# Kernel optimization log

Measured on AMD Instinct MI355X. Metric: run time of the kernel, lower is better.

## Reference

```python
import jax, jax.numpy as jnp
import numpy as np

N_QUBITS = 8
N_LAYERS = 2
LN_EPS = 1e-5


def _ry(theta):
    # RY(t) = [[cos t/2, -sin t/2],[sin t/2, cos t/2]]; works batched or scalar
    c = jnp.cos(theta * 0.5)
    s = jnp.sin(theta * 0.5)
    return jnp.stack([jnp.stack([c, -s], -1), jnp.stack([s, c], -1)], -2).astype(jnp.complex64)


def _rz(theta):
    # RZ(t) = diag(e^{-it/2}, e^{it/2})
    e = jnp.exp(-0.5j * theta.astype(jnp.complex64))
    z = jnp.zeros_like(e)
    return jnp.stack([jnp.stack([e, z], -1), jnp.stack([z, jnp.conj(e)], -1)], -2)


def _apply_1q(psi, U, wire):
    # psi: (B, 2,...,2) with wire 0 most significant (PennyLane convention)
    ax = wire + 1
    psi = jnp.moveaxis(psi, ax, 1)
    psi = jnp.einsum('bpq,bq...->bp...', U, psi)
    return jnp.moveaxis(psi, 1, ax)


def _apply_cnot(psi, c, t):
    ca, ta = c + 1, t + 1
    psi = jnp.moveaxis(psi, (ca, ta), (1, 2))  # (B, 2c, 2t, rest)
    psi = jnp.stack([psi[:, 0], psi[:, 1, ::-1]], axis=1)  # flip target where control=1
    return jnp.moveaxis(psi, (1, 2), (ca, ta))


def _quantum(feats, q_weights):
    # feats: (B, 8) angle-encoded features; q_weights: (2, 8, 3)
    B = feats.shape[0]
    f = feats.astype(jnp.float32)
    psi = jnp.zeros((B,) + (2,) * N_QUBITS, jnp.complex64)
    psi = psi.at[(slice(None),) + (0,) * N_QUBITS].set(1.0)
    for l in range(N_LAYERS):
        for i in range(N_QUBITS):
            # gate order on wire i: RY(f_i), RZ(w0), RY(w1), RZ(w2)
            C = _rz(q_weights[l, i, 2]) @ _ry(q_weights[l, i, 1]) @ _rz(q_weights[l, i, 0])
            U = jnp.einsum('pq,bqr->bpr', C, _ry(f[:, i]))  # (B,2,2)
            psi = _apply_1q(psi, U, i)
        for i in range(N_QUBITS):
            psi = _apply_cnot(psi, i, (i + 1) % N_QUBITS)
    probs = jnp.abs(psi) ** 2  # (B, 2,...,2)
    zs = []
    for i in range(N_QUBITS):
        p = jnp.moveaxis(probs, i + 1, 1).reshape(B, 2, -1).sum(-1)
        zs.append(p[:, 0] - p[:, 1])  # <Z_i> = P(0) - P(1)
    return jnp.stack(zs, -1)  # (B, 8)


def setup_inputs() -> dict:
    key = jax.random.key(0)
    ks = jax.random.split(key, 12)
    B, D, H = 16384, 768, 256
    s = lambda fan_in: 1.0 / np.sqrt(fan_in)
    return {
        'x': jax.random.normal(ks[0], (B, D), jnp.float32),
        'W1': jax.random.uniform(ks[1], (D, H), jnp.float32, -s(D), s(D)),
        'b1': jax.random.uniform(ks[2], (H,), jnp.float32, -s(D), s(D)),
        'W2': jax.random.uniform(ks[3], (H, N_QUBITS), jnp.float32, -s(H), s(H)),
        'b2': jax.random.uniform(ks[4], (N_QUBITS,), jnp.float32, -s(H), s(H)),
        'q_weights': jax.random.normal(ks[5], (N_LAYERS, N_QUBITS, 3), jnp.float32) * 0.01,
        'W3': jax.random.uniform(ks[6], (N_QUBITS, H), jnp.float32, -s(N_QUBITS), s(N_QUBITS)),
        'b3': jax.random.uniform(ks[7], (H,), jnp.float32, -s(N_QUBITS), s(N_QUBITS)),
        'W4': jax.random.uniform(ks[8], (H, D), jnp.float32, -s(H), s(H)),
        'b4': jax.random.uniform(ks[9], (D,), jnp.float32, -s(H), s(H)),
        'gamma': jnp.ones((D,), jnp.float32),
        'beta': jnp.zeros((D,), jnp.float32),
    }


def reference(x, W1, b1, W2, b2, q_weights, W3, b3, W4, b4, gamma, beta):
    # classical compress (dropout = identity in eval)
    h = jax.nn.gelu(x @ W1 + b1, approximate=False)
    feats = h @ W2 + b2  # (B, 8) angle encoding
    z = _quantum(feats, q_weights)  # (B, 8) Pauli-Z expectations
    e = jax.nn.gelu(z @ W3 + b3, approximate=False)
    expanded = e @ W4 + b4
    y = x + expanded
    mu = y.mean(-1, keepdims=True)
    var = y.var(-1, keepdims=True)
    return gamma * (y - mu) / jnp.sqrt(var + LN_EPS) + beta
```

## Files before the change

kernel.cpp:

```cpp
#include <hip/hip_runtime.h>
#include <hip/hip_bf16.h>
#include <math.h>


typedef __attribute__((ext_vector_type(8))) short bf16x8;
typedef __attribute__((ext_vector_type(4))) float f32x4;

__device__ __forceinline__ float gelu_f(float x) {
    return 0.5f * x * (1.0f + erff(x * 0.70710678118654752f));
}

__device__ __forceinline__ short f2b(float x) {
    __hip_bfloat16 h = __float2bfloat16(x);
    return reinterpret_cast<short&>(h);
}

__device__ __forceinline__ short4 f4_to_b4(float4 v) {
    return make_short4(f2b(v.x), f2b(v.y), f2b(v.z), f2b(v.w));
}

__global__ __launch_bounds__(256) void transpose_bf16_kernel(
    const float* __restrict__ in, short* __restrict__ out, int K, int N)
{
    __shared__ float tl[32][33];
    const int k0 = blockIdx.y * 32, n0 = blockIdx.x * 32;
    const int r = threadIdx.x >> 3, c4 = (threadIdx.x & 7) * 4;
    const float4 v = *(const float4*)(in + (size_t)(k0 + r) * N + n0 + c4);
    tl[r][c4] = v.x; tl[r][c4 + 1] = v.y; tl[r][c4 + 2] = v.z; tl[r][c4 + 3] = v.w;
    __syncthreads();
    short4 o = make_short4(f2b(tl[c4][r]), f2b(tl[c4 + 1][r]),
                           f2b(tl[c4 + 2][r]), f2b(tl[c4 + 3][r]));
    *(short4*)(out + (size_t)(n0 + r) * K + k0 + c4) = o;
}

__global__ __launch_bounds__(256) void setup_kernel(
    const float* __restrict__ qw, const float* __restrict__ W2,
    float* __restrict__ Cg, short* __restrict__ W2T)
{
    const int t = threadIdx.x;
    if (t < 16) {
        const float w0 = qw[t * 3 + 0];
        const float w1 = qw[t * 3 + 1];
        const float w2 = qw[t * 3 + 2];
        const float a0 = 0.5f * w0, a2 = 0.5f * w2;
        float s1, c1; sincosf(0.5f * w1, &s1, &c1);
        float sp, cp; sincosf(a0 + a2, &sp, &cp);
        float sm, cm; sincosf(a0 - a2, &sm, &cm);
        Cg[t * 8 + 0] =  c1 * cp;  Cg[t * 8 + 1] = -c1 * sp;
        Cg[t * 8 + 2] = -s1 * cm;  Cg[t * 8 + 3] = -s1 * sm;
        Cg[t * 8 + 4] =  s1 * cm;  Cg[t * 8 + 5] = -s1 * sm;
        Cg[t * 8 + 6] =  c1 * cp;  Cg[t * 8 + 7] =  c1 * sp;
    }
    for (int idx = t; idx < 16 * 256; idx += 256) {
        const int n = idx & 15, k = idx >> 4;
        W2T[(size_t)n * 256 + k] = (n < 8) ? f2b(W2[(size_t)k * 8 + n]) : (short)0;
    }
}

__global__ __launch_bounds__(512) void gemm1_feats_kernel(
    const float* __restrict__ x, const short* __restrict__ W1bt,
    const float* __restrict__ b1, const short* __restrict__ W2T,
    const float* __restrict__ b2, float* __restrict__ feats, int M)
{
    __shared__ short As[2][64][40];
    __shared__ short hb[64][264];

    const int tid = threadIdx.x;
    const int wid = tid >> 6, L = tid & 63;
    const int quad = L >> 4, r16 = L & 15;
    const int mw = wid & 1, nw = wid >> 1;
    const int m0 = blockIdx.x * 64;

    const int m_s = tid >> 3, k_s = (tid & 7) << 2;
    const float* xp = x + (size_t)(m0 + m_s) * 768 + k_s;

    const short* bp = W1bt + (size_t)(nw * 64 + r16) * 768 + quad * 8;

    f32x4 acc[2][4];
    #pragma unroll
    for (int i = 0; i < 2; ++i)
        #pragma unroll
        for (int j = 0; j < 4; ++j) acc[i][j] = (f32x4){0.f, 0.f, 0.f, 0.f};

    float4 v0 = *(const float4*)(xp);
    *(short4*)&As[0][m_s][k_s] = f4_to_b4(v0);
    float4 v1 = *(const float4*)(xp + 32);
    __syncthreads();

    for (int kt = 0; kt < 24; ++kt) {
        const int buf = kt & 1;
        float4 vn = v1;
        if (kt + 2 < 24) vn = *(const float4*)(xp + (kt + 2) * 32);

        const bf16x8 a0 = *(const bf16x8*)&As[buf][32 * mw + r16][quad * 8];
        const bf16x8 a1 = *(const bf16x8*)&As[buf][32 * mw + 16 + r16][quad * 8];
        #pragma unroll
        for (int nt = 0; nt < 4; ++nt) {
            const bf16x8 bfr = *(const bf16x8*)(bp + (size_t)nt * 16 * 768 + kt * 32);
            acc[0][nt] = __builtin_amdgcn_mfma_f32_16x16x32_bf16(a0, bfr, acc[0][nt], 0, 0, 0);
            acc[1][nt] = __builtin_amdgcn_mfma_f32_16x16x32_bf16(a1, bfr, acc[1][nt], 0, 0, 0);
        }
        if (kt + 1 < 24) {
            *(short4*)&As[buf ^ 1][m_s][k_s] = f4_to_b4(v1);
        }
        __syncthreads();
        v1 = vn;
    }

    #pragma unroll
    for (int mt = 0; mt < 2; ++mt) {
        #pragma unroll
        for (int nt = 0; nt < 4; ++nt) {
            const int n = nw * 64 + nt * 16 + r16;
            const float bv = b1[n];
            #pragma unroll
            for (int reg = 0; reg < 4; ++reg) {
                const int rrow = 32 * mw + 16 * mt + quad * 4 + reg;
                hb[rrow][n] = f2b(gelu_f(acc[mt][nt][reg] + bv));
            }
        }
    }
    __syncthreads();

    if (wid < 4) {
        const int mt = wid;
        f32x4 fa = (f32x4){0.f, 0.f, 0.f, 0.f};
        #pragma unroll
        for (int kt = 0; kt < 8; ++kt) {
            const bf16x8 ha = *(const bf16x8*)&hb[16 * mt + r16][kt * 32 + quad * 8];
            const bf16x8 wb = *(const bf16x8*)(W2T + (size_t)r16 * 256 + kt * 32 + quad * 8);
            fa = __builtin_amdgcn_mfma_f32_16x16x32_bf16(ha, wb, fa, 0, 0, 0);
        }
        if (r16 < 8) {
            const float bv = b2[r16];
            #pragma unroll
            for (int reg = 0; reg < 4; ++reg) {
                const int row = m0 + 16 * mt + quad * 4 + reg;
                feats[(size_t)row * 8 + r16] = fa[reg] + bv;
            }
        }
    }
}

__global__ __launch_bounds__(256) void quantum_kernel(
    const float* __restrict__ feats, const float* __restrict__ Cg,
    const float* __restrict__ W3, const float* __restrict__ b3,
    short* __restrict__ ebt)
{
    const int t = threadIdx.x;
    const int wid = t >> 6, L = t & 63;
    const int row = blockIdx.x * 4 + wid;

    const float fv = feats[(size_t)row * 8 + (L & 7)];
    float sv, cv;
    sincosf(0.5f * fv, &sv, &cv);
    float cf[8], sf[8];
    #pragma unroll
    for (int w = 0; w < 8; ++w) {
        cf[w] = __shfl(cv, w, 64);
        sf[w] = __shfl(sv, w, 64);
    }

    float re[4], im[4];
    #pragma unroll
    for (int r = 0; r < 4; ++r) { re[r] = 0.0f; im[r] = 0.0f; }
    re[0] = (L == 0) ? 1.0f : 0.0f;

    const int G = L ^ (L >> 1);
    const int mapB = G ^ 48;
    const bool par = __popc(L) & 1;

    #pragma unroll
    for (int l = 0; l < 2; ++l) {
        #pragma unroll
        for (int w = 0; w < 8; ++w) {
            const float* Cw = Cg + (l * 8 + w) * 8;
            const float c0 = Cw[0], c1 = Cw[1], c2 = Cw[2], c3 = Cw[3];
            const float c4 = Cw[4], c5 = Cw[5], c6 = Cw[6], c7 = Cw[7];
            const float U00r = cf[w]*c0 + sf[w]*c2, U00i = cf[w]*c1 + sf[w]*c3;
            const float U01r = cf[w]*c2 - sf[w]*c0, U01i = cf[w]*c3 - sf[w]*c1;
            const float U10r = cf[w]*c4 + sf[w]*c6, U10i = cf[w]*c5 + sf[w]*c7;
            const float U11r = cf[w]*c6 - sf[w]*c4, U11i = cf[w]*c7 - sf[w]*c5;

            if (w <= 5) {
                const int kb = 5 - w;
                const int xm = 1 << kb;
                const bool hi = (L >> kb) & 1;
                const float u0r = hi ? U11r : U00r;
                const float u0i = hi ? U11i : U00i;
                const float u1r = hi ? U10r : U01r;
                const float u1i = hi ? U10i : U01i;
                #pragma unroll
                for (int r = 0; r < 4; ++r) {
                    const float ore = __shfl_xor(re[r], xm, 64);
                    const float oim = __shfl_xor(im[r], xm, 64);
                    const float nre = u0r*re[r] - u0i*im[r] + u1r*ore - u1i*oim;
                    const float nim = u0r*im[r] + u0i*re[r] + u1r*oim + u1i*ore;
                    re[r] = nre; im[r] = nim;
                }
            } else if (w == 6) {
                float nre[4], nim[4];
                #pragma unroll
                for (int p = 0; p < 2; ++p) {
                    nre[p]   = U00r*re[p]-U00i*im[p] + U01r*re[p+2]-U01i*im[p+2];
                    nim[p]   = U00r*im[p]+U00i*re[p] + U01r*im[p+2]+U01i*re[p+2];
                    nre[p+2] = U10r*re[p]-U10i*im[p] + U11r*re[p+2]-U11i*im[p+2];
                    nim[p+2] = U10r*im[p]+U10i*re[p] + U11r*im[p+2]+U11i*re[p+2];
                }
                #pragma unroll
                for (int r = 0; r < 4; ++r) { re[r] = nre[r]; im[r] = nim[r]; }
            } else {
                float nre[4], nim[4];
                #pragma unroll
                for (int p = 0; p < 4; p += 2) {
                    nre[p]   = U00r*re[p]-U00i*im[p] + U01r*re[p+1]-U01i*im[p+1];
                    nim[p]   = U00r*im[p]+U00i*re[p] + U01r*im[p+1]+U01i*re[p+1];
                    nre[p+1] = U10r*re[p]-U10i*im[p] + U11r*re[p+1]-U11i*im[p+1];
                    nim[p+1] = U10r*im[p]+U10i*re[p] + U11r*im[p+1]+U11i*re[p+1];
                }
                #pragma unroll
                for (int r = 0; r < 4; ++r) { re[r] = nre[r]; im[r] = nim[r]; }
            }
        }

        {
            const float s0r = par ? re[2] : re[0], s0i = par ? im[2] : im[0];
            const float s1r = par ? re[3] : re[1], s1i = par ? im[3] : im[1];
            const float s2r = par ? re[1] : re[3], s2i = par ? im[1] : im[3];
            const float s3r = par ? re[0] : re[2], s3i = par ? im[0] : im[2];
            re[0] = __shfl(s0r, G, 64);    im[0] = __shfl(s0i, G, 64);
            re[1] = __shfl(s1r, mapB, 64); im[1] = __shfl(s1i, mapB, 64);
            re[2] = __shfl(s2r, G, 64);    im[2] = __shfl(s2i, G, 64);
            re[3] = __shfl(s3r, mapB, 64); im[3] = __shfl(s3i, mapB, 64);
        }
    }

    const float p0 = re[0]*re[0] + im[0]*im[0];
    const float p1 = re[1]*re[1] + im[1]*im[1];
    const float p2 = re[2]*re[2] + im[2]*im[2];
    const float p3 = re[3]*re[3] + im[3]*im[3];
    const float pt = p0 + p1 + p2 + p3;
    float v[8];
    #pragma unroll
    for (int w = 0; w < 6; ++w) v[w] = ((L >> (5 - w)) & 1) ? -pt : pt;
    v[6] = p0 + p1 - p2 - p3;
    v[7] = p0 - p1 + p2 - p3;
    #pragma unroll
    for (int j = 0; j < 4; ++j) {
        const float send = (L & 1) ? v[j] : v[j + 4];
        const float keep = (L & 1) ? v[j + 4] : v[j];
        v[j] = keep + __shfl_xor(send, 1, 64);
    }
    #pragma unroll
    for (int j = 0; j < 2; ++j) {
        const float send = (L & 2) ? v[j] : v[j + 2];
        const float keep = (L & 2) ? v[j + 2] : v[j];
        v[j] = keep + __shfl_xor(send, 2, 64);
    }
    {
        const float send = (L & 4) ? v[0] : v[1];
        const float keep = (L & 4) ? v[1] : v[0];
        v[0] = keep + __shfl_xor(send, 4, 64);
    }
    v[0] += __shfl_xor(v[0], 8, 64);
    v[0] += __shfl_xor(v[0], 16, 64);
    v[0] += __shfl_xor(v[0], 32, 64);
    float z[8];
    #pragma unroll
    for (int w = 0; w < 8; ++w) {
        const int src = ((w & 1) << 2) | (w & 2) | ((w >> 2) & 1);
        z[w] = __shfl(v[0], src, 64);
    }

    const float4 b3v = *(const float4*)(b3 + 4 * L);
    float acc[4] = {b3v.x, b3v.y, b3v.z, b3v.w};
    #pragma unroll
    for (int w = 0; w < 8; ++w) {
        const float4 w3v = *(const float4*)(W3 + (size_t)w * 256 + 4 * L);
        acc[0] += z[w] * w3v.x; acc[1] += z[w] * w3v.y;
        acc[2] += z[w] * w3v.z; acc[3] += z[w] * w3v.w;
    }
    *(short4*)(ebt + (size_t)row * 256 + 4 * L) =
        make_short4(f2b(gelu_f(acc[0])), f2b(gelu_f(acc[1])),
                    f2b(gelu_f(acc[2])), f2b(gelu_f(acc[3])));
}

__global__ __launch_bounds__(256) void gemm4_ln_kernel(
    const short* __restrict__ ebt, const short* __restrict__ W4bt,
    const float* __restrict__ b4, const float* __restrict__ x,
    const float* __restrict__ gamma, const float* __restrict__ beta,
    float* __restrict__ out, int M)
{
    __shared__ short Ae[16][264];
    __shared__ float red[4][16][2];
    __shared__ float stats[16][2];

    const int tid = threadIdx.x;
    const int wv = tid >> 6, L = tid & 63;
    const int quad = L >> 4, r16 = L & 15;
    const int m0 = blockIdx.x * 16;
    const int n0 = wv * 192;

    {
        const int m_s = tid >> 4, k16 = (tid & 15) * 16;
        const int4* ep = (const int4*)(ebt + (size_t)(m0 + m_s) * 256 + k16);
        const int4 e0 = ep[0], e1 = ep[1];
        *(int4*)&Ae[m_s][k16] = e0;
        *(int4*)&Ae[m_s][k16 + 8] = e1;
    }
    __syncthreads();

    const short* bp = W4bt + (size_t)(n0 + r16) * 256 + quad * 8;

    f32x4 acc[12];
    #pragma unroll
    for (int nt = 0; nt < 12; ++nt) acc[nt] = (f32x4){0.f, 0.f, 0.f, 0.f};

    for (int kt = 0; kt < 8; ++kt) {
        const bf16x8 af = *(const bf16x8*)&Ae[r16][kt * 32 + quad * 8];
        #pragma unroll
        for (int nt = 0; nt < 12; ++nt) {
            const bf16x8 bfr = *(const bf16x8*)(bp + (size_t)nt * 16 * 256 + kt * 32);
            acc[nt] = __builtin_amdgcn_mfma_f32_16x16x32_bf16(af, bfr, acc[nt], 0, 0, 0);
        }
    }

    float ps[4] = {0.f, 0.f, 0.f, 0.f}, pq[4] = {0.f, 0.f, 0.f, 0.f};
    #pragma unroll
    for (int nt = 0; nt < 12; ++nt) {
        const int n = n0 + nt * 16 + r16;
        const float bv = b4[n];
        #pragma unroll
        for (int reg = 0; reg < 4; ++reg) {
            const int row = m0 + quad * 4 + reg;
            const float y = acc[nt][reg] + bv + x[(size_t)row * 768 + n];
            acc[nt][reg] = y;
            ps[reg] += y;
            pq[reg] += y * y;
        }
    }
    #pragma unroll
    for (int off = 1; off < 16; off <<= 1) {
        #pragma unroll
        for (int reg = 0; reg < 4; ++reg) {
            ps[reg] += __shfl_xor(ps[reg], off, 64);
            pq[reg] += __shfl_xor(pq[reg], off, 64);
        }
    }
    if (r16 == 0) {
        #pragma unroll
        for (int reg = 0; reg < 4; ++reg) {
            red[wv][quad * 4 + reg][0] = ps[reg];
            red[wv][quad * 4 + reg][1] = pq[reg];
        }
    }
    __syncthreads();
    if (tid < 16) {
        const float S = red[0][tid][0] + red[1][tid][0] + red[2][tid][0] + red[3][tid][0];
        const float Q = red[0][tid][1] + red[1][tid][1] + red[2][tid][1] + red[3][tid][1];
        const float mu = S * (1.0f / 768.0f);
        const float var = Q * (1.0f / 768.0f) - mu * mu;
        stats[tid][0] = mu;
        stats[tid][1] = rsqrtf(var + 1e-5f);
    }
    __syncthreads();

    float mu_r[4], rs_r[4];
    #pragma unroll
    for (int reg = 0; reg < 4; ++reg) {
        mu_r[reg] = stats[quad * 4 + reg][0];
        rs_r[reg] = stats[quad * 4 + reg][1];
    }
    #pragma unroll
    for (int nt = 0; nt < 12; ++nt) {
        const int n = n0 + nt * 16 + r16;
        const float g = gamma[n], bt = beta[n];
        #pragma unroll
        for (int reg = 0; reg < 4; ++reg) {
            const int row = m0 + quad * 4 + reg;
            out[(size_t)row * 768 + n] = g * (acc[nt][reg] - mu_r[reg]) * rs_r[reg] + bt;
        }
    }
}

extern "C" void kernel_launch(void* const* d_in, const int* in_sizes, int n_in,
                              void* d_out, int out_size, void* d_ws, size_t ws_size,
                              hipStream_t stream) {
    (void)n_in; (void)out_size; (void)ws_size;
    const float* x     = (const float*)d_in[0];
    const float* W1    = (const float*)d_in[1];
    const float* b1    = (const float*)d_in[2];
    const float* W2    = (const float*)d_in[3];
    const float* b2    = (const float*)d_in[4];
    const float* qw    = (const float*)d_in[5];
    const float* W3    = (const float*)d_in[6];
    const float* b3    = (const float*)d_in[7];
    const float* W4    = (const float*)d_in[8];
    const float* b4    = (const float*)d_in[9];
    const float* gamma = (const float*)d_in[10];
    const float* beta  = (const float*)d_in[11];
    float* out = (float*)d_out;

    const int D = 768, H = 256;
    const int B = in_sizes[0] / D;

    short* W1bt  = (short*)d_ws;
    short* W4bt  = W1bt + (size_t)H * D;
    short* W2T   = W4bt + (size_t)D * H;
    float* Cg    = (float*)(W2T + 16 * 256);
    float* feats = Cg + 128;
    short* ebt   = (short*)(feats + (size_t)B * 8);

    transpose_bf16_kernel<<<dim3(H / 32, D / 32), 256, 0, stream>>>(W1, W1bt, D, H);
    transpose_bf16_kernel<<<dim3(D / 32, H / 32), 256, 0, stream>>>(W4, W4bt, H, D);
    setup_kernel<<<1, 256, 0, stream>>>(qw, W2, Cg, W2T);
    gemm1_feats_kernel<<<dim3(B / 64), 512, 0, stream>>>(x, W1bt, b1, W2T, b2, feats, B);
    quantum_kernel<<<dim3(B / 4), 256, 0, stream>>>(feats, Cg, W3, b3, ebt);
    gemm4_ln_kernel<<<dim3(B / 16), 256, 0, stream>>>(ebt, W4bt, b4, x, gamma, beta, out, B);
}
```

Before: 234.1 us.

## Fuse GEMM1, quantum simulation, GEMM4 and LayerNorm into one kernel with split-bf16 activations

Measured after the change: 209.4 us. -10.6%, faster.

```diff
diff --git a/kernel.cpp b/kernel.cpp
--- a/kernel.cpp
+++ b/kernel.cpp
@@ -15,114 +15,153 @@
     return reinterpret_cast<short&>(h);
 }
 
+__device__ __forceinline__ float b2f(short s) {
+    union { unsigned u; float f; } c;
+    c.u = ((unsigned)(unsigned short)s) << 16;
+    return c.f;
+}
+
 __device__ __forceinline__ short4 f4_to_b4(float4 v) {
     return make_short4(f2b(v.x), f2b(v.y), f2b(v.z), f2b(v.w));
 }
 
-__global__ __launch_bounds__(256) void transpose_bf16_kernel(
-    const float* __restrict__ in, short* __restrict__ out, int K, int N)
+__device__ __forceinline__ void split4(float4 v, short4& hi, short4& lo) {
+    hi = f4_to_b4(v);
+    lo = make_short4(f2b(v.x - b2f(hi.x)), f2b(v.y - b2f(hi.y)),
+                     f2b(v.z - b2f(hi.z)), f2b(v.w - b2f(hi.w)));
+}
+
+__global__ __launch_bounds__(256) void prep_kernel(
+    const float* __restrict__ W1, const float* __restrict__ W4,
+    const float* __restrict__ qw, const float* __restrict__ W2,
+    short* __restrict__ W1bt, short* __restrict__ W4bt,
+    short* __restrict__ W2T, float* __restrict__ Cg)
 {
     __shared__ float tl[32][33];
-    const int k0 = blockIdx.y * 32, n0 = blockIdx.x * 32;
-    const int r = threadIdx.x >> 3, c4 = (threadIdx.x & 7) * 4;
-    const float4 v = *(const float4*)(in + (size_t)(k0 + r) * N + n0 + c4);
-    tl[r][c4] = v.x; tl[r][c4 + 1] = v.y; tl[r][c4 + 2] = v.z; tl[r][c4 + 3] = v.w;
-    __syncthreads();
-    short4 o = make_short4(f2b(tl[c4][r]), f2b(tl[c4 + 1][r]),
-                           f2b(tl[c4 + 2][r]), f2b(tl[c4 + 3][r]));
-    *(short4*)(out + (size_t)(n0 + r) * K + k0 + c4) = o;
-}
-
-__global__ __launch_bounds__(256) void setup_kernel(
-    const float* __restrict__ qw, const float* __restrict__ W2,
-    float* __restrict__ Cg, short* __restrict__ W2T)
-{
-    const int t = threadIdx.x;
-    if (t < 16) {
-        const float w0 = qw[t * 3 + 0];
-        const float w1 = qw[t * 3 + 1];
-        const float w2 = qw[t * 3 + 2];
-        const float a0 = 0.5f * w0, a2 = 0.5f * w2;
-        float s1, c1; sincosf(0.5f * w1, &s1, &c1);
-        float sp, cp; sincosf(a0 + a2, &sp, &cp);
-        float sm, cm; sincosf(a0 - a2, &sm, &cm);
-        Cg[t * 8 + 0] =  c1 * cp;  Cg[t * 8 + 1] = -c1 * sp;
-        Cg[t * 8 + 2] = -s1 * cm;  Cg[t * 8 + 3] = -s1 * sm;
-        Cg[t * 8 + 4] =  s1 * cm;  Cg[t * 8 + 5] = -s1 * sm;
-        Cg[t * 8 + 6] =  c1 * cp;  Cg[t * 8 + 7] =  c1 * sp;
+    const int i = blockIdx.x, t = threadIdx.x;
+    if (i < 384) {
+        const float* in; short* outp; int K, N, k0, n0;
+        if (i < 192) {
+            in = W1; outp = W1bt; K = 768; N = 256;
+            k0 = (i >> 3) * 32; n0 = (i & 7) * 32;
+        } else {
+            const int j = i - 192;
+            in = W4; outp = W4bt; K = 256; N = 768;
+            k0 = (j & 7) * 32; n0 = (j >> 3) * 32;
+        }
+        const int r = t >> 3, c4 = (t & 7) * 4;
+        const float4 v = *(const float4*)(in + (size_t)(k0 + r) * N + n0 + c4);
+        tl[r][c4] = v.x; tl[r][c4 + 1] = v.y; tl[r][c4 + 2] = v.z; tl[r][c4 + 3] = v.w;
+        __syncthreads();
+        short4 o = make_short4(f2b(tl[c4][r]), f2b(tl[c4 + 1][r]),
+                               f2b(tl[c4 + 2][r]), f2b(tl[c4 + 3][r]));
+        *(short4*)(outp + (size_t)(n0 + r) * K + k0 + c4) = o;
+    } else {
+        if (t < 16) {
+            const float w0 = qw[t * 3 + 0];
+            const float w1 = qw[t * 3 + 1];
+            const float w2 = qw[t * 3 + 2];
+            const float a0 = 0.5f * w0, a2 = 0.5f * w2;
+            float s1, c1; sincosf(0.5f * w1, &s1, &c1);
+            float sp, cp; sincosf(a0 + a2, &sp, &cp);
+            float sm, cm; sincosf(a0 - a2, &sm, &cm);
+            Cg[t * 8 + 0] =  c1 * cp;  Cg[t * 8 + 1] = -c1 * sp;
+            Cg[t * 8 + 2] = -s1 * cm;  Cg[t * 8 + 3] = -s1 * sm;
+            Cg[t * 8 + 4] =  s1 * cm;  Cg[t * 8 + 5] = -s1 * sm;
+            Cg[t * 8 + 6] =  c1 * cp;  Cg[t * 8 + 7] =  c1 * sp;
+        }
+        for (int idx = t; idx < 16 * 256; idx += 256) {
+            const int n = idx & 15, k = idx >> 4;
+            W2T[(size_t)n * 256 + k] = (n < 8) ? f2b(W2[(size_t)k * 8 + n]) : (short)0;
+        }
     }
-    for (int idx = t; idx < 16 * 256; idx += 256) {
-        const int n = idx & 15, k = idx >> 4;
-        W2T[(size_t)n * 256 + k] = (n < 8) ? f2b(W2[(size_t)k * 8 + n]) : (short)0;
-    }
-}
-
-__global__ __launch_bounds__(512) void gemm1_feats_kernel(
+}
+
+__global__ __launch_bounds__(256, 2) void fused_kernel(
     const float* __restrict__ x, const short* __restrict__ W1bt,
     const float* __restrict__ b1, const short* __restrict__ W2T,
-    const float* __restrict__ b2, float* __restrict__ feats, int M)
+    const float* __restrict__ b2, const float* __restrict__ Cg,
+    const float* __restrict__ W3, const float* __restrict__ b3,
+    const short* __restrict__ W4bt, const float* __restrict__ b4,
+    const float* __restrict__ gamma, const float* __restrict__ beta,
+    float* __restrict__ out)
 {
-    __shared__ short As[2][64][40];
-    __shared__ short hb[64][264];
+    __shared__ short Ash[2][32][40];
+    __shared__ short Asl[2][32][40];
+    __shared__ short hb[32][264];
+    __shared__ short ehi[32][264];
+    __shared__ short elo[32][264];
+    __shared__ float feats_s[32][8];
+    __shared__ float red[4][32][2];
+    __shared__ float stats_s[32][2];
 
     const int tid = threadIdx.x;
     const int wid = tid >> 6, L = tid & 63;
     const int quad = L >> 4, r16 = L & 15;
-    const int mw = wid & 1, nw = wid >> 1;
-    const int m0 = blockIdx.x * 64;
-
-    const int m_s = tid >> 3, k_s = (tid & 7) << 2;
-    const float* xp = x + (size_t)(m0 + m_s) * 768 + k_s;
-
-    const short* bp = W1bt + (size_t)(nw * 64 + r16) * 768 + quad * 8;
-
-    f32x4 acc[2][4];
-    #pragma unroll
-    for (int i = 0; i < 2; ++i)
-        #pragma unroll
-        for (int j = 0; j < 4; ++j) acc[i][j] = (f32x4){0.f, 0.f, 0.f, 0.f};
-
-    float4 v0 = *(const float4*)(xp);
-    *(short4*)&As[0][m_s][k_s] = f4_to_b4(v0);
-    float4 v1 = *(const float4*)(xp + 32);
-    __syncthreads();
-
-    for (int kt = 0; kt < 24; ++kt) {
-        const int buf = kt & 1;
-        float4 vn = v1;
-        if (kt + 2 < 24) vn = *(const float4*)(xp + (kt + 2) * 32);
-
-        const bf16x8 a0 = *(const bf16x8*)&As[buf][32 * mw + r16][quad * 8];
-        const bf16x8 a1 = *(const bf16x8*)&As[buf][32 * mw + 16 + r16][quad * 8];
-        #pragma unroll
-        for (int nt = 0; nt < 4; ++nt) {
-            const bf16x8 bfr = *(const bf16x8*)(bp + (size_t)nt * 16 * 768 + kt * 32);
-            acc[0][nt] = __builtin_amdgcn_mfma_f32_16x16x32_bf16(a0, bfr, acc[0][nt], 0, 0, 0);
-            acc[1][nt] = __builtin_amdgcn_mfma_f32_16x16x32_bf16(a1, bfr, acc[1][nt], 0, 0, 0);
-        }
-        if (kt + 1 < 24) {
-            *(short4*)&As[buf ^ 1][m_s][k_s] = f4_to_b4(v1);
-        }
+    const int m0 = blockIdx.x * 32;
+
+    {
+        const int m_s = tid >> 3, k_s = (tid & 7) << 2;
+        const float* xp = x + (size_t)(m0 + m_s) * 768 + k_s;
+        const short* bp = W1bt + (size_t)(wid * 64 + r16) * 768 + quad * 8;
+
+        f32x4 acc[2][4];
+        #pragma unroll
+        for (int i = 0; i < 2; ++i)
+            #pragma unroll
+            for (int j = 0; j < 4; ++j) acc[i][j] = (f32x4){0.f, 0.f, 0.f, 0.f};
+
+        float4 v0 = *(const float4*)(xp);
+        {
+            short4 hi, lo; split4(v0, hi, lo);
+            *(short4*)&Ash[0][m_s][k_s] = hi;
+            *(short4*)&Asl[0][m_s][k_s] = lo;
+        }
+        float4 v1 = *(const float4*)(xp + 32);
         __syncthreads();
-        v1 = vn;
-    }
-
-    #pragma unroll
-    for (int mt = 0; mt < 2; ++mt) {
-        #pragma unroll
-        for (int nt = 0; nt < 4; ++nt) {
-            const int n = nw * 64 + nt * 16 + r16;
-            const float bv = b1[n];
-            #pragma unroll
-            for (int reg = 0; reg < 4; ++reg) {
-                const int rrow = 32 * mw + 16 * mt + quad * 4 + reg;
-                hb[rrow][n] = f2b(gelu_f(acc[mt][nt][reg] + bv));
+
+        for (int kt = 0; kt < 24; ++kt) {
+            const int buf = kt & 1;
+            float4 vn = v1;
+            if (kt + 2 < 24) vn = *(const float4*)(xp + (kt + 2) * 32);
+
+            const bf16x8 a0h = *(const bf16x8*)&Ash[buf][r16][quad * 8];
+            const bf16x8 a0l = *(const bf16x8*)&Asl[buf][r16][quad * 8];
+            const bf16x8 a1h = *(const bf16x8*)&Ash[buf][16 + r16][quad * 8];
+            const bf16x8 a1l = *(const bf16x8*)&Asl[buf][16 + r16][quad * 8];
+            #pragma unroll
+            for (int nt = 0; nt < 4; ++nt) {
+                const bf16x8 bfr = *(const bf16x8*)(bp + (size_t)nt * 16 * 768 + kt * 32);
+                acc[0][nt] = __builtin_amdgcn_mfma_f32_16x16x32_bf16(a0h, bfr, acc[0][nt], 0, 0, 0);
+                acc[0][nt] = __builtin_amdgcn_mfma_f32_16x16x32_bf16(a0l, bfr, acc[0][nt], 0, 0, 0);
+                acc[1][nt] = __builtin_amdgcn_mfma_f32_16x16x32_bf16(a1h, bfr, acc[1][nt], 0, 0, 0);
+                acc[1][nt] = __builtin_amdgcn_mfma_f32_16x16x32_bf16(a1l, bfr, acc[1][nt], 0, 0, 0);
+            }
+            if (kt + 1 < 24) {
+                short4 hi, lo; split4(v1, hi, lo);
+                *(short4*)&Ash[buf ^ 1][m_s][k_s] = hi;
+                *(short4*)&Asl[buf ^ 1][m_s][k_s] = lo;
+            }
+            __syncthreads();
+            v1 = vn;
+        }
+
+        #pragma unroll
+        for (int mt = 0; mt < 2; ++mt) {
+            #pragma unroll
+            for (int nt = 0; nt < 4; ++nt) {
+                const int n = wid * 64 + nt * 16 + r16;
+                const float bv = b1[n];
+                #pragma unroll
+                for (int reg = 0; reg < 4; ++reg) {
+                    hb[16 * mt + quad * 4 + reg][n] = f2b(gelu_f(acc[mt][nt][reg] + bv));
+                }
             }
         }
     }
     __syncthreads();
 
-    if (wid < 4) {
+    if (wid < 2) {
         const int mt = wid;
         f32x4 fa = (f32x4){0.f, 0.f, 0.f, 0.f};
         #pragma unroll
@@ -135,250 +174,254 @@
             const float bv = b2[r16];
             #pragma unroll
             for (int reg = 0; reg < 4; ++reg) {
-                const int row = m0 + 16 * mt + quad * 4 + reg;
-                feats[(size_t)row * 8 + r16] = fa[reg] + bv;
-            }
-        }
-    }
-}
-
-__global__ __launch_bounds__(256) void quantum_kernel(
-    const float* __restrict__ feats, const float* __restrict__ Cg,
-    const float* __restrict__ W3, const float* __restrict__ b3,
-    short* __restrict__ ebt)
-{
-    const int t = threadIdx.x;
-    const int wid = t >> 6, L = t & 63;
-    const int row = blockIdx.x * 4 + wid;
-
-    const float fv = feats[(size_t)row * 8 + (L & 7)];
-    float sv, cv;
-    sincosf(0.5f * fv, &sv, &cv);
-    float cf[8], sf[8];
-    #pragma unroll
-    for (int w = 0; w < 8; ++w) {
-        cf[w] = __shfl(cv, w, 64);
-        sf[w] = __shfl(sv, w, 64);
-    }
-
-    float re[4], im[4];
-    #pragma unroll
-    for (int r = 0; r < 4; ++r) { re[r] = 0.0f; im[r] = 0.0f; }
-    re[0] = (L == 0) ? 1.0f : 0.0f;
-
-    const int G = L ^ (L >> 1);
-    const int mapB = G ^ 48;
-    const bool par = __popc(L) & 1;
-
-    #pragma unroll
-    for (int l = 0; l < 2; ++l) {
-        #pragma unroll
-        for (int w = 0; w < 8; ++w) {
-            const float* Cw = Cg + (l * 8 + w) * 8;
-            const float c0 = Cw[0], c1 = Cw[1], c2 = Cw[2], c3 = Cw[3];
-            const float c4 = Cw[4], c5 = Cw[5], c6 = Cw[6], c7 = Cw[7];
-            const float U00r = cf[w]*c0 + sf[w]*c2, U00i = cf[w]*c1 + sf[w]*c3;
-            const float U01r = cf[w]*c2 - sf[w]*c0, U01i = cf[w]*c3 - sf[w]*c1;
-            const float U10r = cf[w]*c4 + sf[w]*c6, U10i = cf[w]*c5 + sf[w]*c7;
-            const float U11r = cf[w]*c6 - sf[w]*c4, U11i = cf[w]*c7 - sf[w]*c5;
-
-            if (w <= 5) {
-                const int kb = 5 - w;
-                const int xm = 1 << kb;
-                const bool hi = (L >> kb) & 1;
-                const float u0r = hi ? U11r : U00r;
-                const float u0i = hi ? U11i : U00i;
-                const float u1r = hi ? U10r : U01r;
-                const float u1i = hi ? U10i : U01i;
-                #pragma unroll
-                for (int r = 0; r < 4; ++r) {
-                    const float ore = __shfl_xor(re[r], xm, 64);
-                    const float oim = __shfl_xor(im[r], xm, 64);
-                    const float nre = u0r*re[r] - u0i*im[r] + u1r*ore - u1i*oim;
-                    const float nim = u0r*im[r] + u0i*re[r] + u1r*oim + u1i*ore;
-                    re[r] = nre; im[r] = nim;
-                }
-            } else if (w == 6) {
-                float nre[4], nim[4];
-                #pragma unroll
-                for (int p = 0; p < 2; ++p) {
-                    nre[p]   = U00r*re[p]-U00i*im[p] + U01r*re[p+2]-U01i*im[p+2];
-                    nim[p]   = U00r*im[p]+U00i*re[p] + U01r*im[p+2]+U01i*re[p+2];
-                    nre[p+2] = U10r*re[p]-U10i*im[p] + U11r*re[p+2]-U11i*im[p+2];
-                    nim[p+2] = U10r*im[p]+U10i*re[p] + U11r*im[p+2]+U11i*re[p+2];
-                }
-                #pragma unroll
-                for (int r = 0; r < 4; ++r) { re[r] = nre[r]; im[r] = nim[r]; }
-            } else {
-                float nre[4], nim[4];
-                #pragma unroll
-                for (int p = 0; p < 4; p += 2) {
-                    nre[p]   = U00r*re[p]-U00i*im[p] + U01r*re[p+1]-U01i*im[p+1];
-                    nim[p]   = U00r*im[p]+U00i*re[p] + U01r*im[p+1]+U01i*re[p+1];
-                    nre[p+1] = U10r*re[p]-U10i*im[p] + U11r*re[p+1]-U11i*im[p+1];
-                    nim[p+1] = U10r*im[p]+U10i*re[p] + U11r*im[p+1]+U11i*re[p+1];
-                }
-                #pragma unroll
-                for (int r = 0; r < 4; ++r) { re[r] = nre[r]; im[r] = nim[r]; }
-            }
-        }
-
-        {
-            const float s0r = par ? re[2] : re[0], s0i = par ? im[2] : im[0];
-            const float s1r = par ? re[3] : re[1], s1i = par ? im[3] : im[1];
-            const float s2r = par ? re[1] : re[3], s2i = par ? im[1] : im[3];
-            const float s3r = par ? re[0] : re[2], s3i = par ? im[0] : im[2];
-            re[0] = __shfl(s0r, G, 64);    im[0] = __shfl(s0i, G, 64);
-            re[1] = __shfl(s1r, mapB, 64); im[1] = __shfl(s1i, mapB, 64);
-            re[2] = __shfl(s2r, G, 64);    im[2] = __shfl(s2i, G, 64);
-            re[3] = __shfl(s3r, mapB, 64); im[3] = __shfl(s3i, mapB, 64);
-        }
-    }
-
-    const float p0 = re[0]*re[0] + im[0]*im[0];
-    const float p1 = re[1]*re[1] + im[1]*im[1];
-    const float p2 = re[2]*re[2] + im[2]*im[2];
-    const float p3 = re[3]*re[3] + im[3]*im[3];
-    const float pt = p0 + p1 + p2 + p3;
-    float v[8];
-    #pragma unroll
-    for (int w = 0; w < 6; ++w) v[w] = ((L >> (5 - w)) & 1) ? -pt : pt;
-    v[6] = p0 + p1 - p2 - p3;
-    v[7] = p0 - p1 + p2 - p3;
-    #pragma unroll
-    for (int j = 0; j < 4; ++j) {
-        const float send = (L & 1) ? v[j] : v[j + 4];
-        const float keep = (L & 1) ? v[j + 4] : v[j];
-        v[j] = keep + __shfl_xor(send, 1, 64);
-    }
-    #pragma unroll
-    for (int j = 0; j < 2; ++j) {
-        const float send = (L & 2) ? v[j] : v[j + 2];
-        const float keep = (L & 2) ? v[j + 2] : v[j];
-        v[j] = keep + __shfl_xor(send, 2, 64);
-    }
-    {
-        const float send = (L & 4) ? v[0] : v[1];
-        const float keep = (L & 4) ? v[1] : v[0];
-        v[0] = keep + __shfl_xor(send, 4, 64);
-    }
-    v[0] += __shfl_xor(v[0], 8, 64);
-    v[0] += __shfl_xor(v[0], 16, 64);
-    v[0] += __shfl_xor(v[0], 32, 64);
-    float z[8];
-    #pragma unroll
-    for (int w = 0; w < 8; ++w) {
-        const int src = ((w & 1) << 2) | (w & 2) | ((w >> 2) & 1);
-        z[w] = __shfl(v[0], src, 64);
-    }
-
-    const float4 b3v = *(const float4*)(b3 + 4 * L);
-    float acc[4] = {b3v.x, b3v.y, b3v.z, b3v.w};
-    #pragma unroll
-    for (int w = 0; w < 8; ++w) {
-        const float4 w3v = *(const float4*)(W3 + (size_t)w * 256 + 4 * L);
-        acc[0] += z[w] * w3v.x; acc[1] += z[w] * w3v.y;
-        acc[2] += z[w] * w3v.z; acc[3] += z[w] * w3v.w;
-    }
-    *(short4*)(ebt + (size_t)row * 256 + 4 * L) =
-        make_short4(f2b(gelu_f(acc[0])), f2b(gelu_f(acc[1])),
-                    f2b(gelu_f(acc[2])), f2b(gelu_f(acc[3])));
-}
-
-__global__ __launch_bounds__(256) void gemm4_ln_kernel(
-    const short* __restrict__ ebt, const short* __restrict__ W4bt,
-    const float* __restrict__ b4, const float* __restrict__ x,
-    const float* __restrict__ gamma, const float* __restrict__ beta,
-    float* __restrict__ out, int M)
-{
-    __shared__ short Ae[16][264];
-    __shared__ float red[4][16][2];
-    __shared__ float stats[16][2];
-
-    const int tid = threadIdx.x;
-    const int wv = tid >> 6, L = tid & 63;
-    const int quad = L >> 4, r16 = L & 15;
-    const int m0 = blockIdx.x * 16;
-    const int n0 = wv * 192;
-
-    {
-        const int m_s = tid >> 4, k16 = (tid & 15) * 16;
-        const int4* ep = (const int4*)(ebt + (size_t)(m0 + m_s) * 256 + k16);
-        const int4 e0 = ep[0], e1 = ep[1];
-        *(int4*)&Ae[m_s][k16] = e0;
-        *(int4*)&Ae[m_s][k16 + 8] = e1;
+                feats_s[16 * mt + quad * 4 + reg][r16] = fa[reg] + bv;
+            }
+        }
     }
     __syncthreads();
 
-    const short* bp = W4bt + (size_t)(n0 + r16) * 256 + quad * 8;
-
-    f32x4 acc[12];
-    #pragma unroll
-    for (int nt = 0; nt < 12; ++nt) acc[nt] = (f32x4){0.f, 0.f, 0.f, 0.f};
-
-    for (int kt = 0; kt < 8; ++kt) {
-        const bf16x8 af = *(const bf16x8*)&Ae[r16][kt * 32 + quad * 8];
-        #pragma unroll
-        for (int nt = 0; nt < 12; ++nt) {
-            const bf16x8 bfr = *(const bf16x8*)(bp + (size_t)nt * 16 * 256 + kt * 32);
-            acc[nt] = __builtin_amdgcn_mfma_f32_16x16x32_bf16(af, bfr, acc[nt], 0, 0, 0);
-        }
-    }
-
-    float ps[4] = {0.f, 0.f, 0.f, 0.f}, pq[4] = {0.f, 0.f, 0.f, 0.f};
-    #pragma unroll
-    for (int nt = 0; nt < 12; ++nt) {
-        const int n = n0 + nt * 16 + r16;
-        const float bv = b4[n];
-        #pragma unroll
-        for (int reg = 0; reg < 4; ++reg) {
-            const int row = m0 + quad * 4 + reg;
-            const float y = acc[nt][reg] + bv + x[(size_t)row * 768 + n];
-            acc[nt][reg] = y;
-            ps[reg] += y;
-            pq[reg] += y * y;
-        }
-    }
-    #pragma unroll
-    for (int off = 1; off < 16; off <<= 1) {
-        #pragma unroll
-        for (int reg = 0; reg < 4; ++reg) {
-            ps[reg] += __shfl_xor(ps[reg], off, 64);
-            pq[reg] += __shfl_xor(pq[reg], off, 64);
-        }
-    }
-    if (r16 == 0) {
-        #pragma unroll
-        for (int reg = 0; reg < 4; ++reg) {
-            red[wv][quad * 4 + reg][0] = ps[reg];
-            red[wv][quad * 4 + reg][1] = pq[reg];
+    {
+        float4 w3r[8];
+        #pragma unroll
+        for (int w = 0; w < 8; ++w) w3r[w] = *(const float4*)(W3 + (size_t)w * 256 + 4 * L);
+        const float4 b3v = *(const float4*)(b3 + 4 * L);
+
+        const int G = L ^ (L >> 1);
+        const int mapB = G ^ 48;
+        const bool par = __popc(L) & 1;
+
+        #pragma unroll 1
+        for (int rr = 0; rr < 8; ++rr) {
+            const int row = wid * 8 + rr;
+            const float fv = feats_s[row][L & 7];
+            float sv, cv;
+            sincosf(0.5f * fv, &sv, &cv);
+            float cf[8], sf[8];
+            #pragma unroll
+            for (int w = 0; w < 8; ++w) {
+                cf[w] = __shfl(cv, w, 64);
+                sf[w] = __shfl(sv, w, 64);
+            }
+
+            float re[4], im[4];
+            #pragma unroll
+            for (int r = 0; r < 4; ++r) { re[r] = 0.0f; im[r] = 0.0f; }
+            re[0] = (L == 0) ? 1.0f : 0.0f;
+
+            #pragma unroll
+            for (int l = 0; l < 2; ++l) {
+                #pragma unroll
+                for (int w = 0; w < 8; ++w) {
+                    const float* Cw = Cg + (l * 8 + w) * 8;
+                    const float c0 = Cw[0], c1 = Cw[1], c2 = Cw[2], c3 = Cw[3];
+                    const float c4 = Cw[4], c5 = Cw[5], c6 = Cw[6], c7 = Cw[7];
+                    const float U00r = cf[w]*c0 + sf[w]*c2, U00i = cf[w]*c1 + sf[w]*c3;
+                    const float U01r = cf[w]*c2 - sf[w]*c0, U01i = cf[w]*c3 - sf[w]*c1;
+                    const float U10r = cf[w]*c4 + sf[w]*c6, U10i = cf[w]*c5 + sf[w]*c7;
+                    const float U11r = cf[w]*c6 - sf[w]*c4, U11i = cf[w]*c7 - sf[w]*c5;
+
+                    if (w <= 5) {
+                        const int kb = 5 - w;
+                        const int xm = 1 << kb;
+                        const bool hi = (L >> kb) & 1;
+                        const float u0r = hi ? U11r : U00r;
+                        const float u0i = hi ? U11i : U00i;
+                        const float u1r = hi ? U10r : U01r;
+                        const float u1i = hi ? U10i : U01i;
+                        #pragma unroll
+                        for (int r = 0; r < 4; ++r) {
+                            const float ore = __shfl_xor(re[r], xm, 64);
+                            const float oim = __shfl_xor(im[r], xm, 64);
+                            const float nre = u0r*re[r] - u0i*im[r] + u1r*ore - u1i*oim;
+                            const float nim = u0r*im[r] + u0i*re[r] + u1r*oim + u1i*ore;
+                            re[r] = nre; im[r] = nim;
+                        }
+                    } else if (w == 6) {
+                        float nre[4], nim[4];
+                        #pragma unroll
+                        for (int p = 0; p < 2; ++p) {
+                            nre[p]   = U00r*re[p]-U00i*im[p] + U01r*re[p+2]-U01i*im[p+2];
+                            nim[p]   = U00r*im[p]+U00i*re[p] + U01r*im[p+2]+U01i*re[p+2];
+                            nre[p+2] = U10r*re[p]-U10i*im[p] + U11r*re[p+2]-U11i*im[p+2];
+                            nim[p+2] = U10r*im[p]+U10i*re[p] + U11r*im[p+2]+U11i*re[p+2];
+                        }
+                        #pragma unroll
+                        for (int r = 0; r < 4; ++r) { re[r] = nre[r]; im[r] = nim[r]; }
+                    } else {
+                        float nre[4], nim[4];
+                        #pragma unroll
+                        for (int p = 0; p < 4; p += 2) {
+                            nre[p]   = U00r*re[p]-U00i*im[p] + U01r*re[p+1]-U01i*im[p+1];
+                            nim[p]   = U00r*im[p]+U00i*re[p] + U01r*im[p+1]+U01i*re[p+1];
+                            nre[p+1] = U10r*re[p]-U10i*im[p] + U11r*re[p+1]-U11i*im[p+1];
+                            nim[p+1] = U10r*im[p]+U10i*re[p] + U11r*im[p+1]+U11i*re[p+1];
+                        }
+                        #pragma unroll
+                        for (int r = 0; r < 4; ++r) { re[r] = nre[r]; im[r] = nim[r]; }
+                    }
+                }
+
+                {
+                    const float s0r = par ? re[2] : re[0], s0i = par ? im[2] : im[0];
+                    const float s1r = par ? re[3] : re[1], s1i = par ? im[3] : im[1];
+                    const float s2r = par ? re[1] : re[3], s2i = par ? im[1] : im[3];
+                    const float s3r = par ? re[0] : re[2], s3i = par ? im[0] : im[2];
+                    re[0] = __shfl(s0r, G, 64);    im[0] = __shfl(s0i, G, 64);
+                    re[1] = __shfl(s1r, mapB, 64); im[1] = __shfl(s1i, mapB, 64);
+                    re[2] = __shfl(s2r, G, 64);    im[2] = __shfl(s2i, G, 64);
+                    re[3] = __shfl(s3r, mapB, 64); im[3] = __shfl(s3i, mapB, 64);
+                }
+            }
+
+            const float p0 = re[0]*re[0] + im[0]*im[0];
+            const float p1 = re[1]*re[1] + im[1]*im[1];
+            const float p2 = re[2]*re[2] + im[2]*im[2];
+            const float p3 = re[3]*re[3] + im[3]*im[3];
+            const float pt = p0 + p1 + p2 + p3;
+            float v[8];
+            #pragma unroll
+            for (int w = 0; w < 6; ++w) v[w] = ((L >> (5 - w)) & 1) ? -pt : pt;
+            v[6] = p0 + p1 - p2 - p3;
+            v[7] = p0 - p1 + p2 - p3;
+            #pragma unroll
+            for (int j = 0; j < 4; ++j) {
+                const float send = (L & 1) ? v[j] : v[j + 4];
+                const float keep = (L & 1) ? v[j + 4] : v[j];
+                v[j] = keep + __shfl_xor(send, 1, 64);
+            }
+            #pragma unroll
+            for (int j = 0; j < 2; ++j) {
+                const float send = (L & 2) ? v[j] : v[j + 2];
+                const float keep = (L & 2) ? v[j + 2] : v[j];
+                v[j] = keep + __shfl_xor(send, 2, 64);
+            }
+            {
+                const float send = (L & 4) ? v[0] : v[1];
+                const float keep = (L & 4) ? v[1] : v[0];
+                v[0] = keep + __shfl_xor(send, 4, 64);
+            }
+            v[0] += __shfl_xor(v[0], 8, 64);
+            v[0] += __shfl_xor(v[0], 16, 64);
+            v[0] += __shfl_xor(v[0], 32, 64);
+            float z[8];
+            #pragma unroll
+            for (int w = 0; w < 8; ++w) {
+                const int src = ((w & 1) << 2) | (w & 2) | ((w >> 2) & 1);
+                z[w] = __shfl(v[0], src, 64);
+            }
+
+            float a0 = b3v.x, a1 = b3v.y, a2 = b3v.z, a3 = b3v.w;
+            #pragma unroll
+            for (int w = 0; w < 8; ++w) {
+                a0 += z[w] * w3r[w].x; a1 += z[w] * w3r[w].y;
+                a2 += z[w] * w3r[w].z; a3 += z[w] * w3r[w].w;
+            }
+            const float4 ev = make_float4(gelu_f(a0), gelu_f(a1), gelu_f(a2), gelu_f(a3));
+            short4 hi4, lo4; split4(ev, hi4, lo4);
+            *(short4*)&ehi[row][4 * L] = hi4;
+            *(short4*)&elo[row][4 * L] = lo4;
         }
     }
     __syncthreads();
-    if (tid < 16) {
-        const float S = red[0][tid][0] + red[1][tid][0] + red[2][tid][0] + red[3][tid][0];
-        const float Q = red[0][tid][1] + red[1][tid][1] + red[2][tid][1] + red[3][tid][1];
-        const float mu = S * (1.0f / 768.0f);
-        const float var = Q * (1.0f / 768.0f) - mu * mu;
-        stats[tid][0] = mu;
-        stats[tid][1] = rsqrtf(var + 1e-5f);
-    }
-    __syncthreads();
-
-    float mu_r[4], rs_r[4];
-    #pragma unroll
-    for (int reg = 0; reg < 4; ++reg) {
-        mu_r[reg] = stats[quad * 4 + reg][0];
-        rs_r[reg] = stats[quad * 4 + reg][1];
-    }
-    #pragma unroll
-    for (int nt = 0; nt < 12; ++nt) {
-        const int n = n0 + nt * 16 + r16;
-        const float g = gamma[n], bt = beta[n];
-        #pragma unroll
-        for (int reg = 0; reg < 4; ++reg) {
-            const int row = m0 + quad * 4 + reg;
-            out[(size_t)row * 768 + n] = g * (acc[nt][reg] - mu_r[reg]) * rs_r[reg] + bt;
+
+    {
+        const int n0 = wid * 192;
+        const short* bp4 = W4bt + (size_t)(n0 + r16) * 256 + quad * 8;
+
+        f32x4 acc4[2][12];
+        #pragma unroll
+        for (int mt = 0; mt < 2; ++mt)
+            #pragma unroll
+            for (int nt = 0; nt < 12; ++nt) acc4[mt][nt] = (f32x4){0.f, 0.f, 0.f, 0.f};
+
+        for (int kt = 0; kt < 8; ++kt) {
+            const bf16x8 a0h = *(const bf16x8*)&ehi[r16][kt * 32 + quad * 8];
+            const bf16x8 a0l = *(const bf16x8*)&elo[r16][kt * 32 + quad * 8];
+            const bf16x8 a1h = *(const bf16x8*)&ehi[16 + r16][kt * 32 + quad * 8];
+            const bf16x8 a1l = *(const bf16x8*)&elo[16 + r16][kt * 32 + quad * 8];
+            #pragma unroll
+            for (int nt = 0; nt < 12; ++nt) {
+                const bf16x8 bfr = *(const bf16x8*)(bp4 + (size_t)nt * 16 * 256 + kt * 32);
+                acc4[0][nt] = __builtin_amdgcn_mfma_f32_16x16x32_bf16(a0h, bfr, acc4[0][nt], 0, 0, 0);
+                acc4[0][nt] = __builtin_amdgcn_mfma_f32_16x16x32_bf16(a0l, bfr, acc4[0][nt], 0, 0, 0);
+                acc4[1][nt] = __builtin_amdgcn_mfma_f32_16x16x32_bf16(a1h, bfr, acc4[1][nt], 0, 0, 0);
+                acc4[1][nt] = __builtin_amdgcn_mfma_f32_16x16x32_bf16(a1l, bfr, acc4[1][nt], 0, 0, 0);
+            }
+        }
+
+        float ps[2][4], pq[2][4];
+        #pragma unroll
+        for (int mt = 0; mt < 2; ++mt)
+            #pragma unroll
+            for (int reg = 0; reg < 4; ++reg) { ps[mt][reg] = 0.f; pq[mt][reg] = 0.f; }
+
+        #pragma unroll
+        for (int nt = 0; nt < 12; ++nt) {
+            const int n = n0 + nt * 16 + r16;
+            const float bv = b4[n];
+            #pragma unroll
+            for (int mt = 0; mt < 2; ++mt) {
+                #pragma unroll
+                for (int reg = 0; reg < 4; ++reg) {
+                    const int row = m0 + 16 * mt + quad * 4 + reg;
+                    const float y = acc4[mt][nt][reg] + bv + x[(size_t)row * 768 + n];
+                    acc4[mt][nt][reg] = y;
+                    ps[mt][reg] += y;
+                    pq[mt][reg] += y * y;
+                }
+            }
+        }
+        #pragma unroll
+        for (int off = 1; off < 16; off <<= 1) {
+            #pragma unroll
+            for (int mt = 0; mt < 2; ++mt)
+                #pragma unroll
+                for (int reg = 0; reg < 4; ++reg) {
+                    ps[mt][reg] += __shfl_xor(ps[mt][reg], off, 64);
+                    pq[mt][reg] += __shfl_xor(pq[mt][reg], off, 64);
+                }
+        }
+        if (r16 == 0) {
+            #pragma unroll
+            for (int mt = 0; mt < 2; ++mt)
+                #pragma unroll
+                for (int reg = 0; reg < 4; ++reg) {
+                    red[wid][16 * mt + quad * 4 + reg][0] = ps[mt][reg];
+                    red[wid][16 * mt + quad * 4 + reg][1] = pq[mt][reg];
+                }
+        }
+        __syncthreads();
+        if (tid < 32) {
+            const float S = red[0][tid][0] + red[1][tid][0] + red[2][tid][0] + red[3][tid][0];
+            const float Q = red[0][tid][1] + red[1][tid][1] + red[2][tid][1] + red[3][tid][1];
+            const float mu = S * (1.0f / 768.0f);
+            const float var = Q * (1.0f / 768.0f) - mu * mu;
+            stats_s[tid][0] = mu;
+            stats_s[tid][1] = rsqrtf(var + 1e-5f);
+        }
+        __syncthreads();
+
+        float mu_r[2][4], rs_r[2][4];
+        #pragma unroll
+        for (int mt = 0; mt < 2; ++mt)
+            #pragma unroll
+            for (int reg = 0; reg < 4; ++reg) {
+                mu_r[mt][reg] = stats_s[16 * mt + quad * 4 + reg][0];
+                rs_r[mt][reg] = stats_s[16 * mt + quad * 4 + reg][1];
+            }
+        #pragma unroll
+        for (int nt = 0; nt < 12; ++nt) {
+            const int n = n0 + nt * 16 + r16;
+            const float g = gamma[n], bt = beta[n];
+            #pragma unroll
+            for (int mt = 0; mt < 2; ++mt) {
+                #pragma unroll
+                for (int reg = 0; reg < 4; ++reg) {
+                    const int row = m0 + 16 * mt + quad * 4 + reg;
+                    out[(size_t)row * 768 + n] =
+                        g * (acc4[mt][nt][reg] - mu_r[mt][reg]) * rs_r[mt][reg] + bt;
+                }
+            }
         }
     }
 }
@@ -401,20 +444,15 @@
     const float* beta  = (const float*)d_in[11];
     float* out = (float*)d_out;
 
-    const int D = 768, H = 256;
+    const int D = 768;
     const int B = in_sizes[0] / D;
 
-    short* W1bt  = (short*)d_ws;
-    short* W4bt  = W1bt + (size_t)H * D;
-    short* W2T   = W4bt + (size_t)D * H;
-    float* Cg    = (float*)(W2T + 16 * 256);
-    float* feats = Cg + 128;
-    short* ebt   = (short*)(feats + (size_t)B * 8);
-
-    transpose_bf16_kernel<<<dim3(H / 32, D / 32), 256, 0, stream>>>(W1, W1bt, D, H);
-    transpose_bf16_kernel<<<dim3(D / 32, H / 32), 256, 0, stream>>>(W4, W4bt, H, D);
-    setup_kernel<<<1, 256, 0, stream>>>(qw, W2, Cg, W2T);
-    gemm1_feats_kernel<<<dim3(B / 64), 512, 0, stream>>>(x, W1bt, b1, W2T, b2, feats, B);
-    quantum_kernel<<<dim3(B / 4), 256, 0, stream>>>(feats, Cg, W3, b3, ebt);
-    gemm4_ln_kernel<<<dim3(B / 16), 256, 0, stream>>>(ebt, W4bt, b4, x, gamma, beta, out, B);
-}
+    short* W1bt = (short*)d_ws;
+    short* W4bt = W1bt + (size_t)256 * 768;
+    short* W2T  = W4bt + (size_t)768 * 256;
+    float* Cg   = (float*)(W2T + 16 * 256);
+
+    prep_kernel<<<dim3(385), 256, 0, stream>>>(W1, W4, qw, W2, W1bt, W4bt, W2T, Cg);
+    fused_kernel<<<dim3(B / 32), 256, 0, stream>>>(
+        x, W1bt, b1, W2T, b2, Cg, W3, b3, W4bt, b4, gamma, beta, out);
+}
```
